# Performance work log

Hardware: AMD Instinct MI355X
Metric: run time of the kernel (lower is better)

## Reference

```python
import jax, jax.numpy as jnp
import numpy as np

B, T, C, H = 8, 2048, 768, 64  # batch, seq, n_embed, head_size

def setup_inputs() -> dict:
    key = jax.random.key(0)
    kx, kq, kk, kv = jax.random.split(key, 4)
    x = jax.random.normal(kx, (B, T, C), dtype=jnp.float32)
    Wq = jax.random.normal(kq, (C, H), dtype=jnp.float32) * (C ** -0.5)
    Wk = jax.random.normal(kk, (C, H), dtype=jnp.float32) * (C ** -0.5)
    Wv = jax.random.normal(kv, (C, H), dtype=jnp.float32) * (C ** -0.5)
    return {"x": x, "Wq": Wq, "Wk": Wk, "Wv": Wv}

def reference(x, Wq, Wk, Wv):
    # projections (bias-free linears)
    q = jnp.einsum('btc,ch->bth', x, Wq)
    k = jnp.einsum('btc,ch->bth', x, Wk)
    v = jnp.einsum('btc,ch->bth', x, Wv)
    scale = k.shape[-1] ** -0.5
    wei = jnp.einsum('bth,bsh->bts', q, k) * scale  # [B, T, T]
    Tq = x.shape[1]
    causal = jnp.tril(jnp.ones((Tq, Tq), dtype=bool))
    wei = jnp.where(causal, wei, -jnp.inf)
    wei = jax.nn.softmax(wei, axis=-1)
    # dropout p=0.0 -> identity
    out = jnp.einsum('bts,bsh->bth', wei, v)
    return out
```

## Files before the change

### kernel.cpp

```cpp
#include <hip/hip_runtime.h>


typedef __bf16 bf16x8 __attribute__((ext_vector_type(8)));
typedef float  f32x4  __attribute__((ext_vector_type(4)));
typedef unsigned int u32;

union ABu {
    bf16x8 v;
    uint4  u;
    unsigned short us[8];
};

__device__ __forceinline__ unsigned short f2bf(float f) {
    union { float f; unsigned int u; } c; c.f = f;
    unsigned int u = c.u + 0x7fffu + ((c.u >> 16) & 1u);
    return (unsigned short)(u >> 16);
}

__device__ __forceinline__ void gld16(void* lds, const void* g) {
    __builtin_amdgcn_global_load_lds(
        (const u32 __attribute__((address_space(1)))*)g,
        (u32 __attribute__((address_space(3)))*)lds, 16, 0, 0);
}

__global__ __launch_bounds__(256)
void wt_kernel(const float* __restrict__ Wq, const float* __restrict__ Wk,
               const float* __restrict__ Wv, unsigned short* __restrict__ wF) {
    const int j   = blockIdx.x / 6;
    const int kgg = blockIdx.x % 6;
    const int t = threadIdx.x;
    const int kg = kgg * 4 + (t >> 6);
    const int lane = t & 63, quad = lane >> 4, l16 = lane & 15;
    const int m = j >> 2, nb = (j & 3) * 16;
    const float* W = (m == 0) ? Wq : (m == 1) ? Wk : Wv;
    ABu o;
#pragma unroll
    for (int i = 0; i < 8; ++i)
        o.us[i] = f2bf(W[(kg * 32 + quad * 8 + i) * 64 + nb + l16]);
    *(uint4*)(wF + ((size_t)(j * 24 + kg) * 64 + lane) * 8) = o.u;
}

__global__ __launch_bounds__(256)
void qkv_kernel(const float* __restrict__ x, const unsigned short* __restrict__ wF,
                unsigned short* __restrict__ qF, unsigned short* __restrict__ kF,
                unsigned short* __restrict__ vF) {
    __shared__ float          xs[32][68];
    __shared__ unsigned short wsW[24][64][8];
    __shared__ unsigned short Cst[2][12][16][17];
    const int tid  = threadIdx.x;
    const int lane = tid & 63, w = tid >> 6;
    const int l16  = lane & 15, quad = lane >> 4;
    const int mh   = w & 1, nh = w >> 1;
    const int m0   = blockIdx.x * 32;
    const int b    = m0 >> 11;

    f32x4 acc[6];
#pragma unroll
    for (int j = 0; j < 6; ++j) acc[j] = (f32x4){0.f, 0.f, 0.f, 0.f};

    const int xrow = tid >> 4, xc16 = tid & 15;

    for (int kk = 0; kk < 12; ++kk) {
        __syncthreads();
#pragma unroll
        for (int i = 0; i < 6; ++i) {
            const int p = w * 6 + i;
            const int j = p >> 1, kg2 = p & 1;
            gld16((char*)wsW + (size_t)p * 1024 + lane * 16,
                  (const char*)wF + ((size_t)(j * 24 + kk * 2 + kg2) * 64 + lane) * 16);
        }
        float4 xa = *(const float4*)&x[(size_t)(m0 + xrow) * 768 + kk * 64 + xc16 * 4];
        float4 xb = *(const float4*)&x[(size_t)(m0 + 16 + xrow) * 768 + kk * 64 + xc16 * 4];
        *(float4*)&xs[xrow][xc16 * 4]      = xa;
        *(float4*)&xs[16 + xrow][xc16 * 4] = xb;
        __syncthreads();

#pragma unroll
        for (int kg2 = 0; kg2 < 2; ++kg2) {
            const float* xr = &xs[mh * 16 + l16][kg2 * 32 + quad * 8];
            float4 f0 = *(const float4*)xr;
            float4 f1 = *(const float4*)(xr + 4);
            ABu af;
            af.us[0] = f2bf(f0.x); af.us[1] = f2bf(f0.y);
            af.us[2] = f2bf(f0.z); af.us[3] = f2bf(f0.w);
            af.us[4] = f2bf(f1.x); af.us[5] = f2bf(f1.y);
            af.us[6] = f2bf(f1.z); af.us[7] = f2bf(f1.w);
#pragma unroll
            for (int jl = 0; jl < 6; ++jl) {
                const int j = nh * 6 + jl;
                ABu bf;
                bf.u = *(const uint4*)((char*)wsW + (size_t)(j * 2 + kg2) * 1024 + lane * 16);
                acc[jl] = __builtin_amdgcn_mfma_f32_16x16x32_bf16(af.v, bf.v, acc[jl], 0, 0, 0);
            }
        }
    }

    __syncthreads();
#pragma unroll
    for (int jl = 0; jl < 6; ++jl)
#pragma unroll
        for (int r = 0; r < 4; ++r)
            Cst[mh][nh * 6 + jl][quad * 4 + r][l16] = f2bf(acc[jl][r]);
    __syncthreads();

    {
        const int mhh = tid >> 7, kg = (tid >> 6) & 1;
        const int el = tid & 63, eq = el >> 4, e16 = el & 15;
        ABu oq, ok;
#pragma unroll
        for (int i = 0; i < 8; ++i) {
            const int h = kg * 32 + eq * 8 + i;
            oq.us[i] = Cst[mhh][h >> 4][e16][h & 15];
            ok.us[i] = Cst[mhh][4 + (h >> 4)][e16][h & 15];
        }
        const size_t tt = (size_t)b * 128 + ((m0 & 2047) >> 4) + mhh;
        *(uint4*)(qF + ((tt * 2 + kg) * 64 + el) * 8) = oq.u;
        *(uint4*)(kF + ((tt * 2 + kg) * 64 + el) * 8) = ok.u;
    }
    {
        const int nt = tid >> 6;
        const int el = tid & 63, eq = el >> 4, e16 = el & 15;
        const int sv = (m0 & 2047) >> 6, kg = (m0 >> 5) & 1;
        ABu ov;
#pragma unroll
        for (int i = 0; i < 8; ++i) {
            const int loc = eq * 8 + i;
            ov.us[i] = Cst[loc >> 4][8 + nt][loc & 15][e16];
        }
        *(uint4*)(vF + ((((size_t)(b * 32 + sv) * 4 + nt) * 2 + kg) * 64 + el) * 8) = ov.u;
    }
}

__global__ __launch_bounds__(256)
void attn_kernel(const unsigned short* __restrict__ qF,
                 const unsigned short* __restrict__ kF,
                 const unsigned short* __restrict__ vF,
                 float* __restrict__ out, float* __restrict__ lacc) {
    __shared__ unsigned short KS[8][64][8];
    __shared__ unsigned short VS[8][64][8];
    __shared__ unsigned short PT[4][64][20];
    const int tid  = threadIdx.x;
    const int lane = tid & 63, w = tid >> 6;
    const int l16  = lane & 15, quad = lane >> 4;
    const int idx  = blockIdx.x;
    const int b    = idx >> 6;
    const int rem  = idx & 63;
    const int jj   = rem >> 1, half = rem & 1;
    const int qb   = (jj & 1) ? (31 - (jj >> 1)) : (jj >> 1);
    const int tt   = qb * 4 + w;
    const int tq0  = tt * 16;
    const float L2E = 1.44269504089f;
    const float MFIX = 16.0f;

    ABu aq[2];
#pragma unroll
    for (int kg = 0; kg < 2; ++kg)
        aq[kg].u = *(const uint4*)(qF + ((((size_t)b * 128 + tt) * 2 + kg) * 64 + lane) * 8);

    f32x4 acc[4];
#pragma unroll
    for (int nt = 0; nt < 4; ++nt) acc[nt] = (f32x4){0.f, 0.f, 0.f, 0.f};
    float lrow[4] = {0.f, 0.f, 0.f, 0.f};

    for (int st = half; st <= qb; st += 2) {
        const int s0 = st * 64;
        __syncthreads();
        const char* ksrc = (const char*)(kF + (size_t)(b * 128 + st * 4) * 2 * 512);
        const char* vsrc = (const char*)(vF + (size_t)(b * 32 + st) * 4 * 2 * 512);
#pragma unroll
        for (int ii = 0; ii < 2; ++ii) {
            const size_t off = (size_t)w * 2048 + ii * 1024 + lane * 16;
            gld16((char*)KS + off, ksrc + off);
            gld16((char*)VS + off, vsrc + off);
        }
        __syncthreads();

        float p[4][4];
#pragma unroll
        for (int nt = 0; nt < 4; ++nt) {
            ABu k0, k1;
            k0.u = *(const uint4*)((char*)KS + (size_t)(nt * 2 + 0) * 1024 + lane * 16);
            k1.u = *(const uint4*)((char*)KS + (size_t)(nt * 2 + 1) * 1024 + lane * 16);
            f32x4 s = (f32x4){0.f, 0.f, 0.f, 0.f};
            s = __builtin_amdgcn_mfma_f32_16x16x32_bf16(aq[0].v, k0.v, s, 0, 0, 0);
            s = __builtin_amdgcn_mfma_f32_16x16x32_bf16(aq[1].v, k1.v, s, 0, 0, 0);
            const int sg = s0 + nt * 16 + l16;
#pragma unroll
            for (int r = 0; r < 4; ++r) {
                float sc = (sg > tq0 + quad * 4 + r) ? -1e30f : s[r] * 0.125f;
                float pv = exp2f((sc - MFIX) * L2E);
                p[nt][r] = pv;
                lrow[r] += pv;
            }
        }
#pragma unroll
        for (int nt = 0; nt < 4; ++nt) {
            ushort4 pw;
            pw.x = f2bf(p[nt][0]); pw.y = f2bf(p[nt][1]);
            pw.z = f2bf(p[nt][2]); pw.w = f2bf(p[nt][3]);
            *(ushort4*)&PT[w][nt * 16 + l16][quad * 4] = pw;
        }
        ABu ap[2];
#pragma unroll
        for (int ks = 0; ks < 2; ++ks)
#pragma unroll
            for (int j = 0; j < 8; ++j)
                ap[ks].us[j] = PT[w][ks * 32 + quad * 8 + j][l16];
#pragma unroll
        for (int nt = 0; nt < 4; ++nt) {
            ABu v0, v1;
            v0.u = *(const uint4*)((char*)VS + (size_t)(nt * 2 + 0) * 1024 + lane * 16);
            v1.u = *(const uint4*)((char*)VS + (size_t)(nt * 2 + 1) * 1024 + lane * 16);
            acc[nt] = __builtin_amdgcn_mfma_f32_16x16x32_bf16(ap[0].v, v0.v, acc[nt], 0, 0, 0);
            acc[nt] = __builtin_amdgcn_mfma_f32_16x16x32_bf16(ap[1].v, v1.v, acc[nt], 0, 0, 0);
        }
    }

#pragma unroll
    for (int off = 1; off <= 8; off <<= 1)
#pragma unroll
        for (int r = 0; r < 4; ++r)
            lrow[r] += __shfl_xor(lrow[r], off);

    float* obase = out + (size_t)(b * 2048 + tq0) * 64;
#pragma unroll
    for (int nt = 0; nt < 4; ++nt)
#pragma unroll
        for (int r = 0; r < 4; ++r)
            atomicAdd(&obase[(size_t)(quad * 4 + r) * 64 + nt * 16 + l16], acc[nt][r]);
    if (l16 == 0) {
#pragma unroll
        for (int r = 0; r < 4; ++r)
            atomicAdd(&lacc[(size_t)b * 2048 + tq0 + quad * 4 + r], lrow[r]);
    }
}

__global__ __launch_bounds__(256)
void finalize_kernel(float* __restrict__ out, const float* __restrict__ lacc) {
    const int idx = blockIdx.x * 256 + threadIdx.x;
    float4 v = ((float4*)out)[idx];
    const float li = 1.f / lacc[idx >> 4];
    v.x *= li; v.y *= li; v.z *= li; v.w *= li;
    ((float4*)out)[idx] = v;
}

extern "C" void kernel_launch(void* const* d_in, const int* in_sizes, int n_in,
                              void* d_out, int out_size, void* d_ws, size_t ws_size,
                              hipStream_t stream) {
    const float* x  = (const float*)d_in[0];
    const float* Wq = (const float*)d_in[1];
    const float* Wk = (const float*)d_in[2];
    const float* Wv = (const float*)d_in[3];
    float* out = (float*)d_out;

    char* ws = (char*)d_ws;
    unsigned short* wF   = (unsigned short*)ws;
    unsigned short* qF   = (unsigned short*)(ws + (512 << 10));
    unsigned short* kF   = (unsigned short*)(ws + (512 << 10) + (2 << 20));
    unsigned short* vF   = (unsigned short*)(ws + (512 << 10) + (4 << 20));
    float*          lacc = (float*)(ws + (512 << 10) + (6 << 20));

    wt_kernel<<<72, 256, 0, stream>>>(Wq, Wk, Wv, wF);
    hipMemsetAsync(out, 0, (size_t)8 * 2048 * 64 * 4, stream);
    hipMemsetAsync(lacc, 0, (size_t)8 * 2048 * 4, stream);
    qkv_kernel<<<512, 256, 0, stream>>>(x, wF, qF, kF, vF);
    attn_kernel<<<512, 256, 0, stream>>>(qF, kF, vF, out, lacc);
    finalize_kernel<<<1024, 256, 0, stream>>>(out, lacc);
}
```

Before: 131.7 us.

## Split attention KV into four partials, drop LDS staging and atomics

The attention kernel now splits each query block's key range four ways instead of two, running 1024 blocks. Each block writes its own partial output and row sum to a workspace instead of using atomicAdd, and finalize sums the four partials before normalising. K/V fragments are loaded straight from global memory into registers instead of staged through LDS with barriers, which removes the two memsets and the synchronisation. The QKV projection uses 512 threads per block, each wave owning half as many output tiles, with launch bounds added for occupancy. In exchange it adds extra partial-buffer traffic and repeated global loads of K/V per wave.

```diff
diff --git a/kernel.cpp b/kernel.cpp
--- a/kernel.cpp
+++ b/kernel.cpp
@@ -40,7 +40,7 @@
     *(uint4*)(wF + ((size_t)(j * 24 + kg) * 64 + lane) * 8) = o.u;
 }
 
-__global__ __launch_bounds__(256)
+__global__ __launch_bounds__(512, 4)
 void qkv_kernel(const float* __restrict__ x, const unsigned short* __restrict__ wF,
                 unsigned short* __restrict__ qF, unsigned short* __restrict__ kF,
                 unsigned short* __restrict__ vF) {
@@ -54,25 +54,23 @@
     const int m0   = blockIdx.x * 32;
     const int b    = m0 >> 11;
 
-    f32x4 acc[6];
-#pragma unroll
-    for (int j = 0; j < 6; ++j) acc[j] = (f32x4){0.f, 0.f, 0.f, 0.f};
+    f32x4 acc[3];
+#pragma unroll
+    for (int j = 0; j < 3; ++j) acc[j] = (f32x4){0.f, 0.f, 0.f, 0.f};
 
     const int xrow = tid >> 4, xc16 = tid & 15;
 
     for (int kk = 0; kk < 12; ++kk) {
         __syncthreads();
 #pragma unroll
-        for (int i = 0; i < 6; ++i) {
-            const int p = w * 6 + i;
-            const int j = p >> 1, kg2 = p & 1;
-            gld16((char*)wsW + (size_t)p * 1024 + lane * 16,
+        for (int i = 0; i < 3; ++i) {
+            const int c = w * 3 + i;
+            const int j = c >> 1, kg2 = c & 1;
+            gld16((char*)wsW + (size_t)c * 1024 + lane * 16,
                   (const char*)wF + ((size_t)(j * 24 + kk * 2 + kg2) * 64 + lane) * 16);
         }
-        float4 xa = *(const float4*)&x[(size_t)(m0 + xrow) * 768 + kk * 64 + xc16 * 4];
-        float4 xb = *(const float4*)&x[(size_t)(m0 + 16 + xrow) * 768 + kk * 64 + xc16 * 4];
-        *(float4*)&xs[xrow][xc16 * 4]      = xa;
-        *(float4*)&xs[16 + xrow][xc16 * 4] = xb;
+        *(float4*)&xs[xrow][xc16 * 4] =
+            *(const float4*)&x[(size_t)(m0 + xrow) * 768 + kk * 64 + xc16 * 4];
         __syncthreads();
 
 #pragma unroll
@@ -86,8 +84,8 @@
             af.us[4] = f2bf(f1.x); af.us[5] = f2bf(f1.y);
             af.us[6] = f2bf(f1.z); af.us[7] = f2bf(f1.w);
 #pragma unroll
-            for (int jl = 0; jl < 6; ++jl) {
-                const int j = nh * 6 + jl;
+            for (int jl = 0; jl < 3; ++jl) {
+                const int j = nh * 3 + jl;
                 ABu bf;
                 bf.u = *(const uint4*)((char*)wsW + (size_t)(j * 2 + kg2) * 1024 + lane * 16);
                 acc[jl] = __builtin_amdgcn_mfma_f32_16x16x32_bf16(af.v, bf.v, acc[jl], 0, 0, 0);
@@ -97,15 +95,16 @@
 
     __syncthreads();
 #pragma unroll
-    for (int jl = 0; jl < 6; ++jl)
-#pragma unroll
-        for (int r = 0; r < 4; ++r)
-            Cst[mh][nh * 6 + jl][quad * 4 + r][l16] = f2bf(acc[jl][r]);
+    for (int jl = 0; jl < 3; ++jl)
+#pragma unroll
+        for (int r = 0; r < 4; ++r)
+            Cst[mh][nh * 3 + jl][quad * 4 + r][l16] = f2bf(acc[jl][r]);
     __syncthreads();
 
-    {
-        const int mhh = tid >> 7, kg = (tid >> 6) & 1;
-        const int el = tid & 63, eq = el >> 4, e16 = el & 15;
+    const int g = tid >> 6, el = tid & 63;
+    const int eq = el >> 4, e16 = el & 15;
+    if (g < 4) {
+        const int mhh = g >> 1, kg = g & 1;
         ABu oq, ok;
 #pragma unroll
         for (int i = 0; i < 8; ++i) {
@@ -116,10 +115,8 @@
         const size_t tt = (size_t)b * 128 + ((m0 & 2047) >> 4) + mhh;
         *(uint4*)(qF + ((tt * 2 + kg) * 64 + el) * 8) = oq.u;
         *(uint4*)(kF + ((tt * 2 + kg) * 64 + el) * 8) = ok.u;
-    }
-    {
-        const int nt = tid >> 6;
-        const int el = tid & 63, eq = el >> 4, e16 = el & 15;
+    } else {
+        const int nt = g & 3;
         const int sv = (m0 & 2047) >> 6, kg = (m0 >> 5) & 1;
         ABu ov;
 #pragma unroll
@@ -131,23 +128,21 @@
     }
 }
 
-__global__ __launch_bounds__(256)
+__global__ __launch_bounds__(256, 4)
 void attn_kernel(const unsigned short* __restrict__ qF,
                  const unsigned short* __restrict__ kF,
                  const unsigned short* __restrict__ vF,
-                 float* __restrict__ out, float* __restrict__ lacc) {
-    __shared__ unsigned short KS[8][64][8];
-    __shared__ unsigned short VS[8][64][8];
+                 float* __restrict__ opart, float* __restrict__ lpart) {
     __shared__ unsigned short PT[4][64][20];
     const int tid  = threadIdx.x;
     const int lane = tid & 63, w = tid >> 6;
     const int l16  = lane & 15, quad = lane >> 4;
     const int idx  = blockIdx.x;
-    const int b    = idx >> 6;
-    const int rem  = idx & 63;
-    const int jj   = rem >> 1, half = rem & 1;
-    const int qb   = (jj & 1) ? (31 - (jj >> 1)) : (jj >> 1);
-    const int tt   = qb * 4 + w;
+    const int b    = idx >> 7;
+    const int rem  = idx & 127;
+    const int jj   = rem >> 2, quarter = rem & 3;
+    const int qs   = (jj & 1) ? (31 - (jj >> 1)) : (jj >> 1);
+    const int tt   = qs * 4 + w;
     const int tq0  = tt * 16;
     const float L2E = 1.44269504089f;
     const float MFIX = 16.0f;
@@ -162,28 +157,20 @@
     for (int nt = 0; nt < 4; ++nt) acc[nt] = (f32x4){0.f, 0.f, 0.f, 0.f};
     float lrow[4] = {0.f, 0.f, 0.f, 0.f};
 
-    for (int st = half; st <= qb; st += 2) {
+    for (int st = quarter; st <= qs; st += 4) {
         const int s0 = st * 64;
-        __syncthreads();
-        const char* ksrc = (const char*)(kF + (size_t)(b * 128 + st * 4) * 2 * 512);
-        const char* vsrc = (const char*)(vF + (size_t)(b * 32 + st) * 4 * 2 * 512);
-#pragma unroll
-        for (int ii = 0; ii < 2; ++ii) {
-            const size_t off = (size_t)w * 2048 + ii * 1024 + lane * 16;
-            gld16((char*)KS + off, ksrc + off);
-            gld16((char*)VS + off, vsrc + off);
-        }
-        __syncthreads();
-
+        const unsigned short* kbase = kF + (size_t)(b * 128 + st * 4) * 2 * 512;
+        const unsigned short* vbase = vF + (size_t)(b * 32 + st) * 8 * 512;
+        ABu kf[8];
+#pragma unroll
+        for (int c = 0; c < 8; ++c)
+            kf[c].u = *(const uint4*)(kbase + (size_t)c * 512 + lane * 8);
         float p[4][4];
 #pragma unroll
         for (int nt = 0; nt < 4; ++nt) {
-            ABu k0, k1;
-            k0.u = *(const uint4*)((char*)KS + (size_t)(nt * 2 + 0) * 1024 + lane * 16);
-            k1.u = *(const uint4*)((char*)KS + (size_t)(nt * 2 + 1) * 1024 + lane * 16);
             f32x4 s = (f32x4){0.f, 0.f, 0.f, 0.f};
-            s = __builtin_amdgcn_mfma_f32_16x16x32_bf16(aq[0].v, k0.v, s, 0, 0, 0);
-            s = __builtin_amdgcn_mfma_f32_16x16x32_bf16(aq[1].v, k1.v, s, 0, 0, 0);
+            s = __builtin_amdgcn_mfma_f32_16x16x32_bf16(aq[0].v, kf[nt * 2 + 0].v, s, 0, 0, 0);
+            s = __builtin_amdgcn_mfma_f32_16x16x32_bf16(aq[1].v, kf[nt * 2 + 1].v, s, 0, 0, 0);
             const int sg = s0 + nt * 16 + l16;
 #pragma unroll
             for (int r = 0; r < 4; ++r) {
@@ -193,6 +180,10 @@
                 lrow[r] += pv;
             }
         }
+        ABu vf[8];
+#pragma unroll
+        for (int c = 0; c < 8; ++c)
+            vf[c].u = *(const uint4*)(vbase + (size_t)c * 512 + lane * 8);
 #pragma unroll
         for (int nt = 0; nt < 4; ++nt) {
             ushort4 pw;
@@ -208,11 +199,8 @@
                 ap[ks].us[j] = PT[w][ks * 32 + quad * 8 + j][l16];
 #pragma unroll
         for (int nt = 0; nt < 4; ++nt) {
-            ABu v0, v1;
-            v0.u = *(const uint4*)((char*)VS + (size_t)(nt * 2 + 0) * 1024 + lane * 16);
-            v1.u = *(const uint4*)((char*)VS + (size_t)(nt * 2 + 1) * 1024 + lane * 16);
-            acc[nt] = __builtin_amdgcn_mfma_f32_16x16x32_bf16(ap[0].v, v0.v, acc[nt], 0, 0, 0);
-            acc[nt] = __builtin_amdgcn_mfma_f32_16x16x32_bf16(ap[1].v, v1.v, acc[nt], 0, 0, 0);
+            acc[nt] = __builtin_amdgcn_mfma_f32_16x16x32_bf16(ap[0].v, vf[nt * 2 + 0].v, acc[nt], 0, 0, 0);
+            acc[nt] = __builtin_amdgcn_mfma_f32_16x16x32_bf16(ap[1].v, vf[nt * 2 + 1].v, acc[nt], 0, 0, 0);
         }
     }
 
@@ -222,24 +210,33 @@
         for (int r = 0; r < 4; ++r)
             lrow[r] += __shfl_xor(lrow[r], off);
 
-    float* obase = out + (size_t)(b * 2048 + tq0) * 64;
+    float* obase = opart + ((size_t)(quarter * 8 + b) * 2048 + tq0) * 64;
 #pragma unroll
     for (int nt = 0; nt < 4; ++nt)
 #pragma unroll
         for (int r = 0; r < 4; ++r)
-            atomicAdd(&obase[(size_t)(quad * 4 + r) * 64 + nt * 16 + l16], acc[nt][r]);
+            obase[(size_t)(quad * 4 + r) * 64 + nt * 16 + l16] = acc[nt][r];
     if (l16 == 0) {
 #pragma unroll
         for (int r = 0; r < 4; ++r)
-            atomicAdd(&lacc[(size_t)b * 2048 + tq0 + quad * 4 + r], lrow[r]);
+            lpart[(size_t)(quarter * 8 + b) * 2048 + tq0 + quad * 4 + r] = lrow[r];
     }
 }
 
 __global__ __launch_bounds__(256)
-void finalize_kernel(float* __restrict__ out, const float* __restrict__ lacc) {
+void finalize_kernel(const float* __restrict__ opart, const float* __restrict__ lpart,
+                     float* __restrict__ out) {
     const int idx = blockIdx.x * 256 + threadIdx.x;
-    float4 v = ((float4*)out)[idx];
-    const float li = 1.f / lacc[idx >> 4];
+    const int row = idx >> 4;
+    float4 v = ((const float4*)opart)[idx];
+    float  l = lpart[row];
+#pragma unroll
+    for (int q = 1; q < 4; ++q) {
+        float4 u = ((const float4*)opart)[(size_t)q * 262144 + idx];
+        v.x += u.x; v.y += u.y; v.z += u.z; v.w += u.w;
+        l += lpart[(size_t)q * 16384 + row];
+    }
+    const float li = 1.f / l;
     v.x *= li; v.y *= li; v.z *= li; v.w *= li;
     ((float4*)out)[idx] = v;
 }
@@ -254,16 +251,15 @@
     float* out = (float*)d_out;
 
     char* ws = (char*)d_ws;
-    unsigned short* wF   = (unsigned short*)ws;
-    unsigned short* qF   = (unsigned short*)(ws + (512 << 10));
-    unsigned short* kF   = (unsigned short*)(ws + (512 << 10) + (2 << 20));
-    unsigned short* vF   = (unsigned short*)(ws + (512 << 10) + (4 << 20));
-    float*          lacc = (float*)(ws + (512 << 10) + (6 << 20));
+    unsigned short* wF    = (unsigned short*)ws;
+    unsigned short* qF    = (unsigned short*)(ws + (512 << 10));
+    unsigned short* kF    = (unsigned short*)(ws + (512 << 10) + (2 << 20));
+    unsigned short* vF    = (unsigned short*)(ws + (512 << 10) + (4 << 20));
+    float*          opart = (float*)(ws + (512 << 10) + (6 << 20));
+    float*          lpart = (float*)(ws + (512 << 10) + (22 << 20));
 
     wt_kernel<<<72, 256, 0, stream>>>(Wq, Wk, Wv, wF);
-    hipMemsetAsync(out, 0, (size_t)8 * 2048 * 64 * 4, stream);
-    hipMemsetAsync(lacc, 0, (size_t)8 * 2048 * 4, stream);
-    qkv_kernel<<<512, 256, 0, stream>>>(x, wF, qF, kF, vF);
-    attn_kernel<<<512, 256, 0, stream>>>(qF, kF, vF, out, lacc);
-    finalize_kernel<<<1024, 256, 0, stream>>>(out, lacc);
-}
+    qkv_kernel<<<512, 512, 0, stream>>>(x, wF, qF, kF, vF);
+    attn_kernel<<<1024, 256, 0, stream>>>(qF, kF, vF, opart, lpart);
+    finalize_kernel<<<1024, 256, 0, stream>>>(opart, lpart, out);
+}
```

Result: no change. 132.4 us (+0.5%).
